# Kernel optimization log

Hardware: AMD Instinct MI355X
Metric: run time of the kernel (lower is better)

Reference implementation:

```python
import jax, jax.numpy as jnp
import numpy as np

HEAD_DIM = 128


def _apply_rotary(x, cos, sin):
    # x: [B, S, H, HD]; cos/sin: [S, HD//2]
    xr = x.reshape(*x.shape[:-1], -1, 2)  # interleaved pairs
    xe, xo = xr[..., 0], xr[..., 1]
    c = cos[None, :, None, :]
    s = sin[None, :, None, :]
    oe = xe * c - xo * s
    oo = xe * s + xo * c
    return jnp.stack([oe, oo], axis=-1).reshape(x.shape)


def setup_inputs() -> dict:
    key = jax.random.key(0)
    ks = jax.random.split(key, 8)
    B, S, D = 2, 1024, 4096
    KVD = 1024  # n_kv_heads * head_dim = 8 * 128
    MAXB, MAXS, KVH, HD = 2, 2048, 8, HEAD_DIM
    theta = 500000.0
    # rotary tables (real/imag of freqs_cis)
    inv = 1.0 / theta ** (np.arange(0, HD, 2)[: HD // 2].astype(np.float32) / HD)
    t = np.arange(S, dtype=np.float32)
    fr = np.outer(t, inv)
    sc = 0.02
    return {
        "x": jax.random.normal(ks[0], (B, S, D), jnp.float32),
        "wq": jax.random.normal(ks[1], (D, D), jnp.float32) * sc,
        "wk": jax.random.normal(ks[2], (D, KVD), jnp.float32) * sc,
        "wv": jax.random.normal(ks[3], (D, KVD), jnp.float32) * sc,
        "wo": jax.random.normal(ks[4], (D, D), jnp.float32) * sc,
        "freqs_cos": jnp.asarray(np.cos(fr)),
        "freqs_sin": jnp.asarray(np.sin(fr)),
        "cache_k": jnp.zeros((MAXB, MAXS, KVH, HD), jnp.float32),
        "cache_v": jnp.zeros((MAXB, MAXS, KVH, HD), jnp.float32),
        "start_pos": 0,
    }


def reference(x, wq, wk, wv, wo, freqs_cos, freqs_sin, cache_k, cache_v, start_pos):
    B, S, D = x.shape
    HD = HEAD_DIM
    H = wq.shape[1] // HD
    KVH = wk.shape[1] // HD
    n_rep = H // KVH

    xq = (x @ wq).reshape(B, S, H, HD)
    xk = (x @ wk).reshape(B, S, KVH, HD)
    xv = (x @ wv).reshape(B, S, KVH, HD)

    xq = _apply_rotary(xq, freqs_cos, freqs_sin)
    xk = _apply_rotary(xk, freqs_cos, freqs_sin)

    # KV-cache update (scatter at start_pos), then read back prefix
    cache_k = cache_k.at[:B, start_pos:start_pos + S].set(xk)
    cache_v = cache_v.at[:B, start_pos:start_pos + S].set(xv)
    keys = cache_k[:B, : start_pos + S]    # [B, T, KVH, HD]
    values = cache_v[:B, : start_pos + S]

    # GQA: repeat kv heads
    keys = jnp.repeat(keys, n_rep, axis=2)      # [B, T, H, HD]
    values = jnp.repeat(values, n_rep, axis=2)

    scale = 1.0 / jnp.sqrt(jnp.float32(HD))
    scores = jnp.einsum("bshd,bthd->bhst", xq, keys) * scale  # [B, H, S, T]

    # causal mask: zeros for the start_pos prefix, upper-triangular -inf after
    T = start_pos + S
    causal = jnp.triu(jnp.full((S, S), -jnp.inf, jnp.float32), k=1)
    mask = jnp.concatenate([jnp.zeros((S, start_pos), jnp.float32), causal], axis=1)  # [S, T]
    scores = scores + mask[None, None, :, :]

    probs = jax.nn.softmax(scores, axis=-1)
    out = jnp.einsum("bhst,bthd->bshd", probs, values).reshape(B, S, D)
    return out @ wo
```

## Files before the change

### kernel.cpp

```cpp
#include <hip/hip_runtime.h>
#include <stdint.h>

#define B_    2
#define S_    1024
#define D_    4096
#define KVD_  1024
#define H_    32
#define KVH_  8
#define HD_   128
#define M_    (B_ * S_)
#define N1_   (D_ + 2 * KVD_)
#define QK_SCALE_L2E (0.08838834764831845f * 1.4426950408889634f)

typedef __attribute__((ext_vector_type(8))) short bf16x8;
typedef __attribute__((ext_vector_type(4))) float f32x4;
typedef __attribute__((ext_vector_type(4))) unsigned short u16x4;
typedef __attribute__((ext_vector_type(8))) unsigned short u16x8;

__device__ inline unsigned short f2bf(float f) {
  unsigned u = __float_as_uint(f);
  u += 0x7FFFu + ((u >> 16) & 1u);
  return (unsigned short)(u >> 16);
}
__device__ inline float bf2f(unsigned short b) {
  return __uint_as_float(((unsigned)b) << 16);
}

#define ASYNC_LD16(g, l) __builtin_amdgcn_global_load_lds( \
    (const __attribute__((address_space(1))) void*)(g),    \
    (__attribute__((address_space(3))) void*)(l), 16, 0, 0)

#define MFMA16(a, b, c) __builtin_amdgcn_mfma_f32_16x16x32_bf16(a, b, c, 0, 0, 0)

#define WAIT_LGKM0() do { asm volatile("s_waitcnt lgkmcnt(0)" ::: "memory"); \
                          __builtin_amdgcn_sched_barrier(0); } while (0)
#define SCHED_PIN() __builtin_amdgcn_sched_barrier(0)
#define BAR() __builtin_amdgcn_s_barrier()

__global__ __launch_bounds__(256) void k_prep(const float* __restrict__ x,
                                              unsigned short* __restrict__ xb,
                                              const float* __restrict__ wq,
                                              const float* __restrict__ wk,
                                              const float* __restrict__ wv,
                                              const float* __restrict__ wo,
                                              unsigned short* __restrict__ w1t,
                                              unsigned short* __restrict__ wot) {
  int bid = blockIdx.x;
  if (bid < 8192) {
    size_t i = ((size_t)bid * 256 + threadIdx.x) * 4;
    float4 v = *(const float4*)(x + i);
    u16x4 o;
    o[0] = f2bf(v.x); o[1] = f2bf(v.y); o[2] = f2bf(v.z); o[3] = f2bf(v.w);
    *(u16x4*)(xb + i) = o;
    return;
  }
  bid -= 8192;
  const float* in; unsigned short* out; int C, bx, by;
  if (bid < 4096)      { in = wq; out = w1t;                          C = 4096; bx = bid & 63; by = bid >> 6; }
  else if (bid < 5120) { bid -= 4096; in = wk; out = w1t + (size_t)D_ * D_;            C = 1024; bx = bid & 15; by = bid >> 4; }
  else if (bid < 6144) { bid -= 5120; in = wv; out = w1t + (size_t)(D_ + KVD_) * D_;   C = 1024; bx = bid & 15; by = bid >> 4; }
  else                 { bid -= 6144; in = wo; out = wot;                              C = 4096; bx = bid & 63; by = bid >> 6; }
  const int R = 4096;
  __shared__ unsigned short tile[64][72];
  int t = threadIdx.x;
  int c0 = bx * 64, r0 = by * 64;
#pragma unroll
  for (int j = 0; j < 4; ++j) {
    int r = (t >> 4) + 16 * j;
    int c = (t & 15) * 4;
    float4 v = *(const float4*)(in + (size_t)(r0 + r) * C + c0 + c);
    tile[r][c + 0] = f2bf(v.x); tile[r][c + 1] = f2bf(v.y);
    tile[r][c + 2] = f2bf(v.z); tile[r][c + 3] = f2bf(v.w);
  }
  __syncthreads();
#pragma unroll
  for (int j = 0; j < 2; ++j) {
    int cc = (t >> 3) + 32 * j;
    int r = (t & 7) * 8;
    u16x8 o;
#pragma unroll
    for (int i = 0; i < 8; ++i) o[i] = tile[r + i][cc];
    *(u16x8*)(out + (size_t)(c0 + cc) * R + r0 + r) = o;
  }
}

__global__ __launch_bounds__(512, 4) void k_gemm_g1(const unsigned short* __restrict__ A,
                                                    const unsigned short* __restrict__ Bt,
                                                    unsigned short* __restrict__ C,
                                                    const float* __restrict__ fc,
                                                    const float* __restrict__ fs) {
  __shared__ unsigned short L[40960];
  const int tid = threadIdx.x, lane = tid & 63, w = tid >> 6;
  const int l15 = lane & 15, l4 = lane >> 4;
  const int wm = w >> 2, wn = w & 3;
  const int brow = blockIdx.y * 128, bcol = blockIdx.x * 192;
  const unsigned short* gA = A + (size_t)brow * 4096;
  const unsigned short* gB = Bt + (size_t)bcol * 4096;
  const int scol = ((lane & 7) ^ (lane >> 3)) * 8;

#define G1_ST_A(bb, kt, r) ASYNC_LD16( \
    gA + (size_t)((r) * 64 + w * 8 + (lane >> 3)) * 4096 + (kt) * 64 + scol, \
    L + (bb) + ((r) * 64 + w * 8) * 64)
#define G1_ST_B(bb, kt, r) ASYNC_LD16( \
    gB + (size_t)((r) * 64 + w * 8 + (lane >> 3)) * 4096 + (kt) * 64 + scol, \
    L + (bb) + 8192 + ((r) * 64 + w * 8) * 64)

  f32x4 acc[4][3] = {};
  bf16x8 bfr[3][2], af[2][2];

  G1_ST_A(0, 0, 0); G1_ST_A(0, 0, 1);
  G1_ST_B(0, 0, 0); G1_ST_B(0, 0, 1); G1_ST_B(0, 0, 2);
  G1_ST_B(20480, 1, 0); G1_ST_B(20480, 1, 1); G1_ST_B(20480, 1, 2);
  asm volatile("s_waitcnt vmcnt(3)" ::: "memory");
  SCHED_PIN();
  BAR();

  for (int t = 0; t < 64; ++t) {
    const int cb = (t & 1) * 20480, nb = cb ^ 20480;

#pragma unroll
    for (int nf = 0; nf < 3; ++nf)
#pragma unroll
      for (int ks = 0; ks < 2; ++ks)
        bfr[nf][ks] = *(const bf16x8*)(L + cb + 8192 +
            (wn * 48 + nf * 16 + l15) * 64 + ((ks * 4 + l4) ^ (l15 & 7)) * 8);
#pragma unroll
    for (int i = 0; i < 2; ++i)
#pragma unroll
      for (int ks = 0; ks < 2; ++ks)
        af[i][ks] = *(const bf16x8*)(L + cb +
            (wm * 64 + i * 16 + l15) * 64 + ((ks * 4 + l4) ^ (l15 & 7)) * 8);
    if (t + 1 < 64) { G1_ST_A(nb, t + 1, 0); G1_ST_A(nb, t + 1, 1); }
    SCHED_PIN(); BAR(); WAIT_LGKM0();
    __builtin_amdgcn_s_setprio(1);
#pragma unroll
    for (int i = 0; i < 2; ++i)
#pragma unroll
      for (int nf = 0; nf < 3; ++nf)
#pragma unroll
        for (int ks = 0; ks < 2; ++ks)
          acc[i][nf] = MFMA16(af[i][ks], bfr[nf][ks], acc[i][nf]);
    __builtin_amdgcn_s_setprio(0);
    BAR();

#pragma unroll
    for (int i = 0; i < 2; ++i)
#pragma unroll
      for (int ks = 0; ks < 2; ++ks)
        af[i][ks] = *(const bf16x8*)(L + cb +
            (wm * 64 + (2 + i) * 16 + l15) * 64 + ((ks * 4 + l4) ^ (l15 & 7)) * 8);
    if (t + 2 < 64) { G1_ST_B(cb, t + 2, 0); G1_ST_B(cb, t + 2, 1); G1_ST_B(cb, t + 2, 2); }
    SCHED_PIN(); BAR(); WAIT_LGKM0();
    __builtin_amdgcn_s_setprio(1);
#pragma unroll
    for (int i = 0; i < 2; ++i)
#pragma unroll
      for (int nf = 0; nf < 3; ++nf)
#pragma unroll
        for (int ks = 0; ks < 2; ++ks)
          acc[2 + i][nf] = MFMA16(af[i][ks], bfr[nf][ks], acc[2 + i][nf]);
    __builtin_amdgcn_s_setprio(0);
    if (t + 2 < 64) { asm volatile("s_waitcnt vmcnt(3)" ::: "memory"); }
    else            { asm volatile("s_waitcnt vmcnt(0)" ::: "memory"); }
    SCHED_PIN();
    BAR();
  }
#undef G1_ST_A
#undef G1_ST_B

#pragma unroll
  for (int mf = 0; mf < 4; ++mf)
#pragma unroll
    for (int nf = 0; nf < 3; ++nf)
#pragma unroll
      for (int q = 0; q < 4; ++q) {
        int row = brow + wm * 64 + mf * 16 + l4 * 4 + q;
        int col = bcol + wn * 48 + nf * 16 + l15;
        float v = acc[mf][nf][q];
        float p = __shfl_xor(v, 1);
        float r;
        if (col < D_ + KVD_) {
          int i = (col & 127) >> 1, s = row & (S_ - 1);
          float c = fc[s * 64 + i], sn = fs[s * 64 + i];
          bool ev = (col & 1) == 0;
          float xe = ev ? v : p, xo = ev ? p : v;
          r = ev ? (xe * c - xo * sn) : (xe * sn + xo * c);
          if (col < D_) r *= QK_SCALE_L2E;
        } else r = v;
        C[(size_t)row * N1_ + col] = f2bf(r);
      }
}

__global__ __launch_bounds__(512, 4) void k_gemm_g2(const unsigned short* __restrict__ A,
                                                    const unsigned short* __restrict__ Bt,
                                                    float* __restrict__ C) {
  __shared__ unsigned short L[32768];
  const int tid = threadIdx.x, lane = tid & 63, w = tid >> 6;
  const int l15 = lane & 15, l4 = lane >> 4;
  const int wm = w >> 2, wn = w & 3;
  const int brow = blockIdx.y * 128, bcol = blockIdx.x * 128;
  const unsigned short* gA = A + (size_t)brow * 4096;
  const unsigned short* gB = Bt + (size_t)bcol * 4096;
  const int scol = ((lane & 7) ^ (lane >> 3)) * 8;

#define G2_ST_A(bb, kt, r) ASYNC_LD16( \
    gA + (size_t)((r) * 64 + w * 8 + (lane >> 3)) * 4096 + (kt) * 64 + scol, \
    L + (bb) + ((r) * 64 + w * 8) * 64)
#define G2_ST_B(bb, kt, r) ASYNC_LD16( \
    gB + (size_t)((r) * 64 + w * 8 + (lane >> 3)) * 4096 + (kt) * 64 + scol, \
    L + (bb) + 8192 + ((r) * 64 + w * 8) * 64)

  f32x4 acc[4][2] = {};
  bf16x8 bfr[2][2], af[2][2];

  G2_ST_A(0, 0, 0); G2_ST_A(0, 0, 1);
  G2_ST_B(0, 0, 0); G2_ST_B(0, 0, 1);
  G2_ST_B(16384, 1, 0); G2_ST_B(16384, 1, 1);
  asm volatile("s_waitcnt vmcnt(2)" ::: "memory");
  SCHED_PIN();
  BAR();

  for (int t = 0; t < 64; ++t) {
    const int cb = (t & 1) * 16384, nb = cb ^ 16384;

#pragma unroll
    for (int nf = 0; nf < 2; ++nf)
#pragma unroll
      for (int ks = 0; ks < 2; ++ks)
        bfr[nf][ks] = *(const bf16x8*)(L + cb + 8192 +
            (wn * 32 + nf * 16 + l15) * 64 + ((ks * 4 + l4) ^ (l15 & 7)) * 8);
#pragma unroll
    for (int i = 0; i < 2; ++i)
#pragma unroll
      for (int ks = 0; ks < 2; ++ks)
        af[i][ks] = *(const bf16x8*)(L + cb +
            (wm * 64 + i * 16 + l15) * 64 + ((ks * 4 + l4) ^ (l15 & 7)) * 8);
    if (t + 1 < 64) { G2_ST_A(nb, t + 1, 0); G2_ST_A(nb, t + 1, 1); }
    SCHED_PIN(); BAR(); WAIT_LGKM0();
    __builtin_amdgcn_s_setprio(1);
#pragma unroll
    for (int i = 0; i < 2; ++i)
#pragma unroll
      for (int nf = 0; nf < 2; ++nf)
#pragma unroll
        for (int ks = 0; ks < 2; ++ks)
          acc[i][nf] = MFMA16(af[i][ks], bfr[nf][ks], acc[i][nf]);
    __builtin_amdgcn_s_setprio(0);
    BAR();

#pragma unroll
    for (int i = 0; i < 2; ++i)
#pragma unroll
      for (int ks = 0; ks < 2; ++ks)
        af[i][ks] = *(const bf16x8*)(L + cb +
            (wm * 64 + (2 + i) * 16 + l15) * 64 + ((ks * 4 + l4) ^ (l15 & 7)) * 8);
    if (t + 2 < 64) { G2_ST_B(cb, t + 2, 0); G2_ST_B(cb, t + 2, 1); }
    SCHED_PIN(); BAR(); WAIT_LGKM0();
    __builtin_amdgcn_s_setprio(1);
#pragma unroll
    for (int i = 0; i < 2; ++i)
#pragma unroll
      for (int nf = 0; nf < 2; ++nf)
#pragma unroll
        for (int ks = 0; ks < 2; ++ks)
          acc[2 + i][nf] = MFMA16(af[i][ks], bfr[nf][ks], acc[2 + i][nf]);
    __builtin_amdgcn_s_setprio(0);
    if (t + 2 < 64) { asm volatile("s_waitcnt vmcnt(2)" ::: "memory"); }
    else            { asm volatile("s_waitcnt vmcnt(0)" ::: "memory"); }
    SCHED_PIN();
    BAR();
  }
#undef G2_ST_A
#undef G2_ST_B

#pragma unroll
  for (int mf = 0; mf < 4; ++mf)
#pragma unroll
    for (int nf = 0; nf < 2; ++nf)
#pragma unroll
      for (int q = 0; q < 4; ++q) {
        int row = brow + wm * 64 + mf * 16 + l4 * 4 + q;
        int col = bcol + wn * 32 + nf * 16 + l15;
        C[(size_t)row * D_ + col] = acc[mf][nf][q];
      }
}

__global__ __launch_bounds__(256) void k_transpose_v(const unsigned short* __restrict__ qkv,
                                                     unsigned short* __restrict__ vt) {
  int bh = blockIdx.z;
  int d0 = blockIdx.x * 64;
  int s0 = blockIdx.y * 64;
  __shared__ unsigned short tile[64][72];
  int t = threadIdx.x;
  const unsigned short* src = qkv + (size_t)(bh >> 3) * S_ * N1_ + D_ + KVD_ + (bh & 7) * HD_;
#pragma unroll
  for (int j = 0; j < 2; ++j) {
    int s = (t >> 3) + 32 * j;
    int d = (t & 7) * 8;
    u16x8 v = *(const u16x8*)(src + (size_t)(s0 + s) * N1_ + d0 + d);
#pragma unroll
    for (int i = 0; i < 8; ++i) tile[s][d + i] = v[i];
  }
  __syncthreads();
#pragma unroll
  for (int j = 0; j < 2; ++j) {
    int d = (t >> 3) + 32 * j;
    int s = (t & 7) * 8;
    u16x8 o;
#pragma unroll
    for (int i = 0; i < 8; ++i) o[i] = tile[s + i][d];
    *(u16x8*)(vt + (size_t)(bh * HD_ + d0 + d) * S_ + s0 + s) = o;
  }
}

__global__ __launch_bounds__(256) void k_flash(const unsigned short* __restrict__ qkv,
                                               const unsigned short* __restrict__ vt,
                                               unsigned short* __restrict__ ao) {
  int f = blockIdx.x;
  int bh = f >> 3;
  int qt = (f & 256) ? (7 - (f & 7)) : (f & 7);
  int b = bh >> 5, h = bh & 31;
  int kh = h >> 2;
  int tid = threadIdx.x, lane = tid & 63, w = tid >> 6;
  int l15 = lane & 15, l4 = lane >> 4;

  __shared__ unsigned short Ks[2 * 64 * 128];
  __shared__ unsigned short Vs[2 * 128 * 64];
  __shared__ unsigned short Ps[4][32 * 64];

  int qb0 = qt * 128;
  int rwb = qb0 + w * 32;
  int NT = 2 * qt + 2;

  const unsigned short* qp = qkv + (size_t)(b * S_ + rwb) * N1_ + h * HD_;
  bf16x8 qf[2][4];
#pragma unroll
  for (int qr = 0; qr < 2; ++qr)
#pragma unroll
    for (int ks = 0; ks < 4; ++ks)
      qf[qr][ks] = *(const bf16x8*)(qp + (size_t)(qr * 16 + l15) * N1_ + ks * 32 + l4 * 8);

  f32x4 o[2][8];
#pragma unroll
  for (int qr = 0; qr < 2; ++qr)
#pragma unroll
    for (int d = 0; d < 8; ++d) o[qr][d] = (f32x4){0.f, 0.f, 0.f, 0.f};
  float lrun[2][4];
#pragma unroll
  for (int qr = 0; qr < 2; ++qr)
#pragma unroll
    for (int q = 0; q < 4; ++q) lrun[qr][q] = 0.f;

  const unsigned short* kbase = qkv + (size_t)(b * S_) * N1_ + D_ + kh * HD_;
  const unsigned short* vbase = vt + (size_t)(b * KVH_ + kh) * HD_ * S_;
  int krl = lane >> 4, kcu = lane & 15;
  int vrl = lane >> 3, vcu = lane & 7;

#define STAGE_KV(bo, itt) do {                                               \
    int kv0s = (itt) * 64;                                                   \
    _Pragma("unroll")                                                        \
    for (int j = 0; j < 4; ++j) {                                            \
      int kc = w * 4 + j;                                                    \
      int krow = kc * 4 + krl;                                               \
      int su = kcu ^ (krow & 7);                                             \
      ASYNC_LD16(kbase + (size_t)(kv0s + krow) * N1_ + su * 8,               \
                 Ks + (bo) * 8192 + kc * 512);                               \
      int vrow = kc * 8 + vrl;                                               \
      int sv = vcu ^ (vrow & 7);                                             \
      ASYNC_LD16(vbase + (size_t)vrow * S_ + kv0s + sv * 8,                  \
                 Vs + (bo) * 8192 + kc * 512);                               \
    }                                                                        \
  } while (0)

  int cur = 0;
  STAGE_KV(0, 0);

  for (int it = 0; it < NT; ++it) {
    int kv0 = it * 64;
    if (it + 1 < NT) {
      STAGE_KV(cur ^ 1, it + 1);
      asm volatile("s_waitcnt vmcnt(8)" ::: "memory");
    } else {
      asm volatile("s_waitcnt vmcnt(0)" ::: "memory");
    }
    __builtin_amdgcn_s_barrier();
    __builtin_amdgcn_sched_barrier(0);

    if (kv0 <= rwb + 31) {
      const unsigned short* Kc = Ks + cur * 8192;
      const unsigned short* Vc = Vs + cur * 8192;

      f32x4 sf[2][4] = {};
      __builtin_amdgcn_s_setprio(1);
#pragma unroll
      for (int ks = 0; ks < 4; ++ks)
#pragma unroll
        for (int n = 0; n < 4; ++n) {
          int row = n * 16 + l15;
          int u = (l4 + ks * 4) ^ (row & 7);
          bf16x8 kf = *(const bf16x8*)(Kc + row * 128 + u * 8);
          sf[0][n] = MFMA16(qf[0][ks], kf, sf[0][n]);
          sf[1][n] = MFMA16(qf[1][ks], kf, sf[1][n]);
        }
      __builtin_amdgcn_s_setprio(0);

      if (kv0 + 63 > rwb) {
#pragma unroll
        for (int qr = 0; qr < 2; ++qr)
#pragma unroll
          for (int n = 0; n < 4; ++n)
#pragma unroll
            for (int q = 0; q < 4; ++q) {
              int rq = rwb + qr * 16 + l4 * 4 + q;
              int ck = kv0 + n * 16 + l15;
              if (ck > rq) sf[qr][n][q] = -1e30f;
            }
      }

#pragma unroll
      for (int qr = 0; qr < 2; ++qr)
#pragma unroll
        for (int n = 0; n < 4; ++n)
#pragma unroll
          for (int q = 0; q < 4; ++q) {
            float p = __builtin_amdgcn_exp2f(sf[qr][n][q]);
            sf[qr][n][q] = p;
            lrun[qr][q] += p;
          }

      unsigned short* pw = Ps[w];
#pragma unroll
      for (int qr = 0; qr < 2; ++qr)
#pragma unroll
        for (int n = 0; n < 4; ++n)
#pragma unroll
          for (int q = 0; q < 4; ++q) {
            int rp = qr * 16 + l4 * 4 + q;
            int cp = n * 16 + l15;
            pw[rp * 64 + (((cp >> 3) ^ (rp & 7)) * 8) + (cp & 7)] = f2bf(sf[qr][n][q]);
          }

      __builtin_amdgcn_s_setprio(1);
#pragma unroll
      for (int kvs = 0; kvs < 2; ++kvs) {
        bf16x8 pa0 = *(const bf16x8*)(pw + (l15) * 64 + (((l4 + kvs * 4) ^ (l15 & 7)) * 8));
        bf16x8 pa1 = *(const bf16x8*)(pw + (16 + l15) * 64 + (((l4 + kvs * 4) ^ (l15 & 7)) * 8));
#pragma unroll
        for (int d = 0; d < 8; ++d) {
          int vrow = d * 16 + l15;
          int u = (l4 + kvs * 4) ^ (vrow & 7);
          bf16x8 vf = *(const bf16x8*)(Vc + vrow * 64 + u * 8);
          o[0][d] = MFMA16(pa0, vf, o[0][d]);
          o[1][d] = MFMA16(pa1, vf, o[1][d]);
        }
      }
      __builtin_amdgcn_s_setprio(0);
    }

    __builtin_amdgcn_s_barrier();
    cur ^= 1;
  }
#undef STAGE_KV

  float invl[2][4];
#pragma unroll
  for (int qr = 0; qr < 2; ++qr)
#pragma unroll
    for (int q = 0; q < 4; ++q) {
      float s = lrun[qr][q];
#pragma unroll
      for (int off = 1; off < 16; off <<= 1) s += __shfl_xor(s, off, 16);
      invl[qr][q] = 1.f / s;
    }
#pragma unroll
  for (int qr = 0; qr < 2; ++qr)
#pragma unroll
    for (int d = 0; d < 8; ++d)
#pragma unroll
      for (int q = 0; q < 4; ++q) {
        int row = b * S_ + rwb + qr * 16 + l4 * 4 + q;
        ao[(size_t)row * D_ + h * HD_ + d * 16 + l15] = f2bf(o[qr][d][q] * invl[qr][q]);
      }
}

extern "C" void kernel_launch(void* const* d_in, const int* in_sizes, int n_in,
                              void* d_out, int out_size, void* d_ws, size_t ws_size,
                              hipStream_t stream) {
  const float* x  = (const float*)d_in[0];
  const float* wq = (const float*)d_in[1];
  const float* wk = (const float*)d_in[2];
  const float* wv = (const float*)d_in[3];
  const float* wo = (const float*)d_in[4];
  const float* fc = (const float*)d_in[5];
  const float* fs = (const float*)d_in[6];
  float* out = (float*)d_out;

  char* ws = (char*)d_ws;
  unsigned short* xb  = (unsigned short*)ws; ws += (size_t)M_ * D_ * 2;
  unsigned short* w1t = (unsigned short*)ws; ws += (size_t)N1_ * D_ * 2;
  unsigned short* wot = (unsigned short*)ws; ws += (size_t)D_ * D_ * 2;
  unsigned short* qkv = (unsigned short*)ws; ws += (size_t)M_ * N1_ * 2;
  unsigned short* vtb = (unsigned short*)ws; ws += (size_t)B_ * KVH_ * HD_ * S_ * 2;
  unsigned short* ao  = (unsigned short*)ws; ws += (size_t)M_ * D_ * 2;

  k_prep<<<18432, 256, 0, stream>>>(x, xb, wq, wk, wv, wo, w1t, wot);

  k_gemm_g1<<<dim3(N1_ / 192, M_ / 128), 512, 0, stream>>>(xb, w1t, qkv, fc, fs);

  k_transpose_v<<<dim3(2, 16, 16), 256, 0, stream>>>(qkv, vtb);
  k_flash<<<dim3(512), 256, 0, stream>>>(qkv, vtb, ao);

  k_gemm_g2<<<dim3(D_ / 128, M_ / 128), 512, 0, stream>>>(ao, wot, out);
}
```

Measured before the change: 263.8 us.

## Move Wo transpose-convert from prep kernel into flash-attention launch as extra blocks

The bf16 transpose-convert of wo no longer runs in k_prep. It now runs as 4096 extra blocks appended to the k_flash grid, reusing the Ks shared buffer as the tile. The aim is to fill idle CUs during the 512-block attention launch, whose causal tiles are unbalanced, and to shorten the prep kernel that sits on the critical path before the first GEMM. The risk is that the transpose blocks compete with attention blocks for bandwidth and scheduling slots. Block dispatch order could also delay attention blocks.

```diff
diff --git a/kernel.cpp b/kernel.cpp
--- a/kernel.cpp
+++ b/kernel.cpp
@@ -42,9 +42,7 @@
                                               const float* __restrict__ wq,
                                               const float* __restrict__ wk,
                                               const float* __restrict__ wv,
-                                              const float* __restrict__ wo,
-                                              unsigned short* __restrict__ w1t,
-                                              unsigned short* __restrict__ wot) {
+                                              unsigned short* __restrict__ w1t) {
   int bid = blockIdx.x;
   if (bid < 8192) {
     size_t i = ((size_t)bid * 256 + threadIdx.x) * 4;
@@ -58,8 +56,7 @@
   const float* in; unsigned short* out; int C, bx, by;
   if (bid < 4096)      { in = wq; out = w1t;                          C = 4096; bx = bid & 63; by = bid >> 6; }
   else if (bid < 5120) { bid -= 4096; in = wk; out = w1t + (size_t)D_ * D_;            C = 1024; bx = bid & 15; by = bid >> 4; }
-  else if (bid < 6144) { bid -= 5120; in = wv; out = w1t + (size_t)(D_ + KVD_) * D_;   C = 1024; bx = bid & 15; by = bid >> 4; }
-  else                 { bid -= 6144; in = wo; out = wot;                              C = 4096; bx = bid & 63; by = bid >> 6; }
+  else                 { bid -= 5120; in = wv; out = w1t + (size_t)(D_ + KVD_) * D_;   C = 1024; bx = bid & 15; by = bid >> 4; }
   const int R = 4096;
   __shared__ unsigned short tile[64][72];
   int t = threadIdx.x;
@@ -315,7 +312,40 @@
 
 __global__ __launch_bounds__(256) void k_flash(const unsigned short* __restrict__ qkv,
                                                const unsigned short* __restrict__ vt,
-                                               unsigned short* __restrict__ ao) {
+                                               unsigned short* __restrict__ ao,
+                                               const float* __restrict__ wo,
+                                               unsigned short* __restrict__ wot) {
+  __shared__ unsigned short Ks[2 * 64 * 128];
+  __shared__ unsigned short Vs[2 * 128 * 64];
+  __shared__ unsigned short Ps[4][32 * 64];
+
+  if (blockIdx.x >= 512) {
+    int wid = blockIdx.x - 512;
+    int bx = wid & 63, by = wid >> 6;
+    unsigned short (*tile)[72] = (unsigned short (*)[72])Ks;
+    int t = threadIdx.x;
+    int c0 = bx * 64, r0 = by * 64;
+#pragma unroll
+    for (int j = 0; j < 4; ++j) {
+      int r = (t >> 4) + 16 * j;
+      int c = (t & 15) * 4;
+      float4 v = *(const float4*)(wo + (size_t)(r0 + r) * 4096 + c0 + c);
+      tile[r][c + 0] = f2bf(v.x); tile[r][c + 1] = f2bf(v.y);
+      tile[r][c + 2] = f2bf(v.z); tile[r][c + 3] = f2bf(v.w);
+    }
+    __syncthreads();
+#pragma unroll
+    for (int j = 0; j < 2; ++j) {
+      int cc = (t >> 3) + 32 * j;
+      int r = (t & 7) * 8;
+      u16x8 o;
+#pragma unroll
+      for (int i = 0; i < 8; ++i) o[i] = tile[r + i][cc];
+      *(u16x8*)(wot + (size_t)(c0 + cc) * 4096 + r0 + r) = o;
+    }
+    return;
+  }
+
   int f = blockIdx.x;
   int bh = f >> 3;
   int qt = (f & 256) ? (7 - (f & 7)) : (f & 7);
@@ -323,10 +353,6 @@
   int kh = h >> 2;
   int tid = threadIdx.x, lane = tid & 63, w = tid >> 6;
   int l15 = lane & 15, l4 = lane >> 4;
-
-  __shared__ unsigned short Ks[2 * 64 * 128];
-  __shared__ unsigned short Vs[2 * 128 * 64];
-  __shared__ unsigned short Ps[4][32 * 64];
 
   int qb0 = qt * 128;
   int rwb = qb0 + w * 32;
@@ -503,12 +529,13 @@
   unsigned short* vtb = (unsigned short*)ws; ws += (size_t)B_ * KVH_ * HD_ * S_ * 2;
   unsigned short* ao  = (unsigned short*)ws; ws += (size_t)M_ * D_ * 2;
 
-  k_prep<<<18432, 256, 0, stream>>>(x, xb, wq, wk, wv, wo, w1t, wot);
+  k_prep<<<14336, 256, 0, stream>>>(x, xb, wq, wk, wv, w1t);
 
   k_gemm_g1<<<dim3(N1_ / 192, M_ / 128), 512, 0, stream>>>(xb, w1t, qkv, fc, fs);
 
   k_transpose_v<<<dim3(2, 16, 16), 256, 0, stream>>>(qkv, vtb);
-  k_flash<<<dim3(512), 256, 0, stream>>>(qkv, vtb, ao);
+
+  k_flash<<<dim3(4608), 256, 0, stream>>>(qkv, vtb, ao, wo, wot);
 
   k_gemm_g2<<<dim3(D_ / 128, M_ / 128), 512, 0, stream>>>(ao, wot, out);
 }
```

After: 275.8 us. +4.5%, slower.
